# Kernel optimization log

Hardware: AMD Instinct MI355X
Metric: run time of the kernel (lower is better)

Reference implementation:

```python
import jax, jax.numpy as jnp
import numpy as np

B, T = 2, 1023
C, H, HS, L, FF = 1024, 16, 64, 6, 4096
V, BS = 50258, 1024


def setup_inputs() -> dict:
    key = jax.random.key(0)
    ks = iter(jax.random.split(key, 80))
    def w(shape):
        return 0.02 * jax.random.normal(next(ks), shape, dtype=jnp.float32)
    inp = {}
    inp['x'] = jax.random.randint(next(ks), (B, T), 0, V)
    inp['y'] = jax.random.randint(next(ks), (B, T), 0, V)
    inp['wte'] = w((V, C))
    inp['wpe_x'] = w((BS, C))
    inp['wpe_y'] = w((BS, C))
    # encoder blocks (stacked over L layers)
    inp['enc_Wq'] = w((L, H, C, HS)); inp['enc_Wk'] = w((L, H, C, HS)); inp['enc_Wv'] = w((L, H, C, HS))
    inp['enc_pw'] = w((L, C, C)); inp['enc_pb'] = jnp.zeros((L, C), jnp.float32)
    inp['enc_ln1g'] = jnp.ones((L, C), jnp.float32); inp['enc_ln1b'] = jnp.zeros((L, C), jnp.float32)
    inp['enc_ln2g'] = jnp.ones((L, C), jnp.float32); inp['enc_ln2b'] = jnp.zeros((L, C), jnp.float32)
    inp['enc_w1'] = w((L, C, FF)); inp['enc_b1'] = jnp.zeros((L, FF), jnp.float32)
    inp['enc_w2'] = w((L, FF, C)); inp['enc_b2'] = jnp.zeros((L, C), jnp.float32)
    # decoder blocks: self-attn (masked), cross-attn, ffn
    inp['dec_sWq'] = w((L, H, C, HS)); inp['dec_sWk'] = w((L, H, C, HS)); inp['dec_sWv'] = w((L, H, C, HS))
    inp['dec_spw'] = w((L, C, C)); inp['dec_spb'] = jnp.zeros((L, C), jnp.float32)
    inp['dec_cWq'] = w((L, H, C, HS)); inp['dec_cWk'] = w((L, H, C, HS)); inp['dec_cWv'] = w((L, H, C, HS))
    inp['dec_cpw'] = w((L, C, C)); inp['dec_cpb'] = jnp.zeros((L, C), jnp.float32)
    inp['dec_ln1g'] = jnp.ones((L, C), jnp.float32); inp['dec_ln1b'] = jnp.zeros((L, C), jnp.float32)
    inp['dec_ln2g'] = jnp.ones((L, C), jnp.float32); inp['dec_ln2b'] = jnp.zeros((L, C), jnp.float32)
    inp['dec_ln3g'] = jnp.ones((L, C), jnp.float32); inp['dec_ln3b'] = jnp.zeros((L, C), jnp.float32)
    inp['dec_w1'] = w((L, C, FF)); inp['dec_b1'] = jnp.zeros((L, FF), jnp.float32)
    inp['dec_w2'] = w((L, FF, C)); inp['dec_b2'] = jnp.zeros((L, C), jnp.float32)
    inp['lnf_g'] = jnp.ones((C,), jnp.float32); inp['lnf_b'] = jnp.zeros((C,), jnp.float32)
    inp['lm_b'] = jnp.zeros((V,), jnp.float32)  # lm_head weight tied to wte
    return inp


def _ln(x, g, b):
    m = x.mean(-1, keepdims=True)
    v = ((x - m) ** 2).mean(-1, keepdims=True)
    return g * (x - m) / jnp.sqrt(v + 1e-5) + b


def _mha(xq, xkv, Wq, Wk, Wv, pw, pb, causal):
    # per-head projections batched over heads: [B,T,C] x [H,C,HS] -> [B,H,T,HS]
    q = jnp.einsum('btc,hcd->bhtd', xq, Wq)
    k = jnp.einsum('bsc,hcd->bhsd', xkv, Wk)
    v = jnp.einsum('bsc,hcd->bhsd', xkv, Wv)
    # NOTE: original scales by sqrt(n_embed) (C from x.size()), not sqrt(head_size)
    s = jnp.einsum('bhtd,bhsd->bhts', q, k) / jnp.sqrt(jnp.float32(C))
    if causal:
        mask = jnp.tril(jnp.ones((xq.shape[1], xkv.shape[1]), bool))
        s = jnp.where(mask, s, -jnp.inf)
    a = jax.nn.softmax(s, axis=-1)
    o = jnp.einsum('bhts,bhsd->bhtd', a, v)
    o = o.transpose(0, 2, 1, 3).reshape(xq.shape[0], xq.shape[1], H * HS)
    return o @ pw + pb


def _ffn(x, w1, b1, w2, b2):
    return jnp.maximum(x @ w1 + b1, 0.0) @ w2 + b2


def _forward(x, y, p):
    enc = p['wte'][x] + p['wpe_x'][:x.shape[1]]
    for i in range(L):
        enc = enc + _ln(_mha(enc, enc, p['enc_Wq'][i], p['enc_Wk'][i], p['enc_Wv'][i], p['enc_pw'][i], p['enc_pb'][i], False), p['enc_ln1g'][i], p['enc_ln1b'][i])
        enc = enc + _ln(_ffn(enc, p['enc_w1'][i], p['enc_b1'][i], p['enc_w2'][i], p['enc_b2'][i]), p['enc_ln2g'][i], p['enc_ln2b'][i])
    dec = p['wte'][y] + p['wpe_y'][:y.shape[1]]
    for i in range(L):
        dec = dec + _ln(_mha(dec, dec, p['dec_sWq'][i], p['dec_sWk'][i], p['dec_sWv'][i], p['dec_spw'][i], p['dec_spb'][i], True), p['dec_ln1g'][i], p['dec_ln1b'][i])
        dec = dec + _ln(_mha(dec, enc, p['dec_cWq'][i], p['dec_cWk'][i], p['dec_cWv'][i], p['dec_cpw'][i], p['dec_cpb'][i], False), p['dec_ln2g'][i], p['dec_ln2b'][i])
        dec = dec + _ln(_ffn(dec, p['dec_w1'][i], p['dec_b1'][i], p['dec_w2'][i], p['dec_b2'][i]), p['dec_ln3g'][i], p['dec_ln3b'][i])
    dec = _ln(dec, p['lnf_g'], p['lnf_b'])
    return dec @ p['wte'].T + p['lm_b']


def reference(x, y, wte, wpe_x, wpe_y,
              enc_Wq, enc_Wk, enc_Wv, enc_pw, enc_pb, enc_ln1g, enc_ln1b, enc_ln2g, enc_ln2b,
              enc_w1, enc_b1, enc_w2, enc_b2,
              dec_sWq, dec_sWk, dec_sWv, dec_spw, dec_spb,
              dec_cWq, dec_cWk, dec_cWv, dec_cpw, dec_cpb,
              dec_ln1g, dec_ln1b, dec_ln2g, dec_ln2b, dec_ln3g, dec_ln3b,
              dec_w1, dec_b1, dec_w2, dec_b2,
              lnf_g, lnf_b, lm_b):
    p = dict(wte=wte, wpe_x=wpe_x, wpe_y=wpe_y,
             enc_Wq=enc_Wq, enc_Wk=enc_Wk, enc_Wv=enc_Wv, enc_pw=enc_pw, enc_pb=enc_pb,
             enc_ln1g=enc_ln1g, enc_ln1b=enc_ln1b, enc_ln2g=enc_ln2g, enc_ln2b=enc_ln2b,
             enc_w1=enc_w1, enc_b1=enc_b1, enc_w2=enc_w2, enc_b2=enc_b2,
             dec_sWq=dec_sWq, dec_sWk=dec_sWk, dec_sWv=dec_sWv, dec_spw=dec_spw, dec_spb=dec_spb,
             dec_cWq=dec_cWq, dec_cWk=dec_cWk, dec_cWv=dec_cWv, dec_cpw=dec_cpw, dec_cpb=dec_cpb,
             dec_ln1g=dec_ln1g, dec_ln1b=dec_ln1b, dec_ln2g=dec_ln2g, dec_ln2b=dec_ln2b,
             dec_ln3g=dec_ln3g, dec_ln3b=dec_ln3b,
             dec_w1=dec_w1, dec_b1=dec_b1, dec_w2=dec_w2, dec_b2=dec_b2,
             lnf_g=lnf_g, lnf_b=lnf_b, lm_b=lm_b)
    return _forward(x, y, p)
```

## Files before the change

kernel.cpp:

```cpp
#include <hip/hip_runtime.h>
#include <hip/hip_bf16.h>

#define BB 2
#define TT 1023
#define CC 1024
#define HH 16
#define HSZ 64
#define LL 6
#define FFD 4096
#define VV 50258
#define MM (BB*TT)
#define MP 2048
#define VP 50304

typedef __attribute__((ext_vector_type(4))) float  f32x4;
typedef __attribute__((ext_vector_type(8))) short  s16x8;
typedef __attribute__((ext_vector_type(4))) short  s16x4;

#define SCHED0   __builtin_amdgcn_sched_barrier(0)
#define SBAR     __builtin_amdgcn_s_barrier()
#define LGKMCNT0 asm volatile("s_waitcnt lgkmcnt(0)" ::: "memory")

__device__ __forceinline__ short f2b(float x) {
    __hip_bfloat16 h = __float2bfloat16(x);
    short s;
    __builtin_memcpy(&s, &h, 2);
    return s;
}

__device__ __forceinline__ void gld16(const void* g, void* l) {
    __builtin_amdgcn_global_load_lds(
        (__attribute__((address_space(1))) const void*)g,
        (__attribute__((address_space(3))) void*)l, 16, 0, 0);
}

__global__ __launch_bounds__(256) void embed_kernel(
    const int* __restrict__ ids, const float* __restrict__ wte,
    const float* __restrict__ wpe, float* __restrict__ out,
    __hip_bfloat16* __restrict__ outb)
{
    int r = blockIdx.x;
    int t = r % TT;
    long id = ids[r];
    int c = threadIdx.x * 4;
    float4 a = *(const float4*)(wte + id * (long)CC + c);
    float4 p = *(const float4*)(wpe + (long)t * CC + c);
    float4 o; o.x = a.x + p.x; o.y = a.y + p.y; o.z = a.z + p.z; o.w = a.w + p.w;
    *(float4*)(out + (long)r * CC + c) = o;
    s16x4 h; h[0] = f2b(o.x); h[1] = f2b(o.y); h[2] = f2b(o.z); h[3] = f2b(o.w);
    *(s16x4*)(outb + (long)r * CC + c) = h;
}

__global__ __launch_bounds__(256) void cvtb_kernel(
    const float* __restrict__ in, __hip_bfloat16* __restrict__ out, long n)
{
    long i = ((long)blockIdx.x * 256 + threadIdx.x) * 8;
    if (i >= n) return;
    float4 f0 = *(const float4*)(in + i);
    float4 f1 = *(const float4*)(in + i + 4);
    s16x8 h;
    h[0]=f2b(f0.x); h[1]=f2b(f0.y); h[2]=f2b(f0.z); h[3]=f2b(f0.w);
    h[4]=f2b(f1.x); h[5]=f2b(f1.y); h[6]=f2b(f1.z); h[7]=f2b(f1.w);
    *(s16x8*)(out + i) = h;
}

__global__ __launch_bounds__(256) void tcvt_kernel(
    const float* __restrict__ in, __hip_bfloat16* __restrict__ out,
    int R, int S, long inZ, long outZa, long outZb, int zdiv)
{
    int z = blockIdx.z;
    in  += (long)z * inZ;
    out += (long)(z / zdiv) * outZa + (long)(z % zdiv) * outZb;
    __shared__ float tile[32][33];
    int s0 = blockIdx.x * 32, r0 = blockIdx.y * 32;
    int tx = threadIdx.x, ty = threadIdx.y;
    #pragma unroll
    for (int i = 0; i < 4; ++i)
        tile[ty + i * 8][tx] = in[(long)(r0 + ty + i * 8) * S + s0 + tx];
    __syncthreads();
    #pragma unroll
    for (int i = 0; i < 4; ++i)
        out[(long)(s0 + ty + i * 8) * R + r0 + tx] =
            __float2bfloat16(tile[tx][ty + i * 8]);
}

template<int WMODE, bool RELU, bool B64>
__global__ __launch_bounds__(256) void mgemm2_kernel(
    const __hip_bfloat16* __restrict__ A, const __hip_bfloat16* __restrict__ B,
    const float* __restrict__ bias, float* __restrict__ Cm,
    __hip_bfloat16* __restrict__ Cb,
    int M, int N, int K, int ldc, int GM)
{
    constexpr int BM   = B64 ? 64 : 128;
    constexpr int ASZ  = BM * 32;
    constexpr int BSZ  = 128 * 32;
    constexpr int BUF  = ASZ + BSZ;
    constexpr int WROW = BM / 2;
    constexpr int NI   = WROW / 16;
    constexpr int NAC  = BM / 64;
    __shared__ short LDS[3 * BUF];

    const int nwg = gridDim.x;
    const int bid = blockIdx.x;
    const int q = nwg >> 3, r = nwg & 7;
    const int xcd = bid & 7, lid = bid >> 3;
    const int swz = (xcd < r) ? xcd * (q + 1) + lid
                              : r * (q + 1) + (xcd - r) * q + lid;
    const int m0 = (swz % GM) * BM;
    const int n0 = (swz / GM) * 128;

    const int tid  = threadIdx.x;
    const int lane = tid & 63, w = tid >> 6;
    const int wr = w >> 1, wc = w & 1;
    const int lr = lane & 15, kg = lane >> 4;

    const __hip_bfloat16* Abase = A + (long)m0 * K;
    const __hip_bfloat16* Bbase = B + (long)n0 * K;

    f32x4 acc[NI][4];
    #pragma unroll
    for (int i = 0; i < NI; ++i)
        #pragma unroll
        for (int j = 0; j < 4; ++j)
            acc[i][j] = (f32x4){0.f, 0.f, 0.f, 0.f};

    const int srow = lane >> 2;
    const int scol = (((lane & 3) ^ ((lane >> 3) & 3))) * 8;

    auto stage = [&](int db, long kofs) {
        short* Ad = &LDS[db * BUF];
        short* Bd = Ad + ASZ;
        #pragma unroll
        for (int p = 0; p < NAC; ++p) {
            int cc = p * 4 + w;
            long ro = (long)(cc * 16 + srow) * K + kofs + scol;
            gld16(Abase + ro, Ad + cc * 512);
        }
        #pragma unroll
        for (int p = 0; p < 2; ++p) {
            int cc = p * 4 + w;
            long ro = (long)(cc * 16 + srow) * K + kofs + scol;
            gld16(Bbase + ro, Bd + cc * 512);
        }
    };
    const int rslot = (kg ^ ((lr >> 1) & 3)) * 8;

    auto compute = [&](int db) {
        const short* Ar = &LDS[db * BUF];
        const short* Br = Ar + ASZ;
        s16x8 af[NI], bf[4];
        #pragma unroll
        for (int i = 0; i < NI; ++i)
            af[i] = *(const s16x8*)&Ar[(wr * WROW + i * 16 + lr) * 32 + rslot];
        #pragma unroll
        for (int j = 0; j < 4; ++j)
            bf[j] = *(const s16x8*)&Br[(wc * 64 + j * 16 + lr) * 32 + rslot];
        __builtin_amdgcn_s_setprio(1);
        #pragma unroll
        for (int i = 0; i < NI; ++i)
            #pragma unroll
            for (int j = 0; j < 4; ++j)
                acc[i][j] = __builtin_amdgcn_mfma_f32_16x16x32_bf16(
                    af[i], bf[j], acc[i][j], 0, 0, 0);
        __builtin_amdgcn_s_setprio(0);
    };

    const int nt = K >> 5;
    stage(0, 0);
    if (nt > 1) stage(1, 32);
    int db = 0;
    for (int t = 0; t < nt; ++t) {
        if (t + 2 < nt) {
            stage((db + 2) % 3, (long)(t + 2) << 5);
            SCHED0;
            if (B64) asm volatile("s_waitcnt vmcnt(6)" ::: "memory");
            else     asm volatile("s_waitcnt vmcnt(8)" ::: "memory");
            SCHED0;
        } else if (t + 1 < nt) {
            SCHED0;
            if (B64) asm volatile("s_waitcnt vmcnt(3)" ::: "memory");
            else     asm volatile("s_waitcnt vmcnt(4)" ::: "memory");
            SCHED0;
        } else {
            SCHED0; asm volatile("s_waitcnt vmcnt(0)" ::: "memory"); SCHED0;
        }
        SBAR; SCHED0;
        compute(db);
        SCHED0; LGKMCNT0; SCHED0; SBAR; SCHED0;
        db = (db + 1) % 3;
    }

    if (WMODE == 0) {
        float* LF = (float*)&LDS[0];
        if (!B64) {
            #pragma unroll
            for (int h = 0; h < 2; ++h) {
                if (wc == h) {
                    #pragma unroll
                    for (int j = 0; j < 4; ++j) {
                        int gcol = n0 + h * 64 + j * 16 + lr;
                        float bv = (bias && gcol < N) ? bias[gcol] : 0.f;
                        #pragma unroll
                        for (int i = 0; i < NI; ++i) {
                            int row0 = wr * WROW + i * 16 + kg * 4;
                            #pragma unroll
                            for (int qq = 0; qq < 4; ++qq) {
                                float v = acc[i][j][qq] + bv;
                                if (RELU) v = fmaxf(v, 0.f);
                                LF[(row0 + qq) * 64 + j * 16 + lr] = v;
                            }
                        }
                    }
                }
                __syncthreads();
                #pragma unroll
                for (int i = 0; i < 16; ++i) {
                    int F = i * 256 + tid;
                    int row = F >> 5, col = (F & 31) * 2;
                    int gr = m0 + row, gc = n0 + h * 64 + col;
                    if (gr < M && gc < N)
                        *(float2*)(Cm + (long)gr * ldc + gc) = *(const float2*)&LF[row * 64 + col];
                }
                __syncthreads();
            }
        } else {
            #pragma unroll
            for (int j = 0; j < 4; ++j) {
                int gcol = n0 + wc * 64 + j * 16 + lr;
                float bv = (bias && gcol < N) ? bias[gcol] : 0.f;
                #pragma unroll
                for (int i = 0; i < NI; ++i) {
                    int row0 = wr * WROW + i * 16 + kg * 4;
                    #pragma unroll
                    for (int qq = 0; qq < 4; ++qq) {
                        float v = acc[i][j][qq] + bv;
                        if (RELU) v = fmaxf(v, 0.f);
                        LF[(row0 + qq) * 128 + wc * 64 + j * 16 + lr] = v;
                    }
                }
            }
            __syncthreads();
            #pragma unroll
            for (int i = 0; i < 16; ++i) {
                int F = i * 256 + tid;
                int row = F >> 6, col = (F & 63) * 2;
                int gr = m0 + row, gc = n0 + col;
                if (gr < M && gc < N)
                    *(float2*)(Cm + (long)gr * ldc + gc) = *(const float2*)&LF[row * 128 + col];
            }
        }
    } else {
        short* LS = (short*)&LDS[0];
        #pragma unroll
        for (int j = 0; j < 4; ++j) {
            int gcol = n0 + wc * 64 + j * 16 + lr;
            float bv = (bias && gcol < N) ? bias[gcol] : 0.f;
            #pragma unroll
            for (int i = 0; i < NI; ++i) {
                int row0 = wr * WROW + i * 16 + kg * 4;
                #pragma unroll
                for (int qq = 0; qq < 4; ++qq) {
                    float v = acc[i][j][qq] + bv;
                    if (RELU) v = fmaxf(v, 0.f);
                    LS[(row0 + qq) * 128 + wc * 64 + j * 16 + lr] = f2b(v);
                }
            }
        }
        __syncthreads();
        #pragma unroll
        for (int i = 0; i < BM / 16; ++i) {
            int F = i * 256 + tid;
            int row = F >> 4, col = (F & 15) * 8;
            int gr = m0 + row, gc = n0 + col;
            if (gr < M && gc < N)
                *(s16x8*)((short*)Cb + (long)gr * ldc + gc) = *(const s16x8*)&LS[row * 128 + col];
        }
    }
}

__global__ __launch_bounds__(256) void mgemm_f32b_kernel(
    const float* __restrict__ A, const float* __restrict__ Bv,
    const float* __restrict__ bias, float* __restrict__ Cm,
    int M, int N, int K, int ldc)
{
    __shared__ short As[128][40];
    __shared__ short Bs[128][40];
    const int tid  = threadIdx.x;
    const int lane = tid & 63, w = tid >> 6;
    const int wr = w >> 1, wc = w & 1;
    const int lr = lane & 15, kg = lane >> 4;
    const int m0 = blockIdx.y * 128, n0 = blockIdx.x * 128;
    const int ar = tid >> 3, ac = (tid & 7) * 4;
    const int br = tid >> 2, bc = (tid & 3) * 8;

    f32x4 acc[4][4];
    #pragma unroll
    for (int i = 0; i < 4; ++i)
        #pragma unroll
        for (int j = 0; j < 4; ++j)
            acc[i][j] = (f32x4){0.f, 0.f, 0.f, 0.f};

    for (int k0 = 0; k0 < K; k0 += 32) {
        #pragma unroll
        for (int p = 0; p < 4; ++p) {
            int row = ar + p * 32, gm = m0 + row;
            float4 f = {0.f, 0.f, 0.f, 0.f};
            if (gm < M) f = *(const float4*)(A + (long)gm * K + k0 + ac);
            s16x4 h; h[0] = f2b(f.x); h[1] = f2b(f.y); h[2] = f2b(f.z); h[3] = f2b(f.w);
            *(s16x4*)&As[row][ac] = h;
        }
        #pragma unroll
        for (int p = 0; p < 2; ++p) {
            int n = br + p * 64, gn = n0 + n;
            s16x8 h = (s16x8){0,0,0,0,0,0,0,0};
            if (gn < N) {
                float4 f0 = *(const float4*)(Bv + (long)gn * K + k0 + bc);
                float4 f1 = *(const float4*)(Bv + (long)gn * K + k0 + bc + 4);
                h[0]=f2b(f0.x); h[1]=f2b(f0.y); h[2]=f2b(f0.z); h[3]=f2b(f0.w);
                h[4]=f2b(f1.x); h[5]=f2b(f1.y); h[6]=f2b(f1.z); h[7]=f2b(f1.w);
            }
            *(s16x8*)&Bs[n][bc] = h;
        }
        __syncthreads();
        s16x8 af[4], bf[4];
        #pragma unroll
        for (int i = 0; i < 4; ++i) af[i] = *(const s16x8*)&As[wr*64 + i*16 + lr][kg*8];
        #pragma unroll
        for (int j = 0; j < 4; ++j) bf[j] = *(const s16x8*)&Bs[wc*64 + j*16 + lr][kg*8];
        #pragma unroll
        for (int i = 0; i < 4; ++i)
            #pragma unroll
            for (int j = 0; j < 4; ++j)
                acc[i][j] = __builtin_amdgcn_mfma_f32_16x16x32_bf16(af[i], bf[j], acc[i][j], 0, 0, 0);
        __syncthreads();
    }
    #pragma unroll
    for (int j = 0; j < 4; ++j) {
        int gcol = n0 + wc * 64 + j * 16 + lr;
        if (gcol >= N) continue;
        float bv = bias ? bias[gcol] : 0.f;
        #pragma unroll
        for (int i = 0; i < 4; ++i) {
            int grow0 = m0 + wr * 64 + i * 16 + kg * 4;
            #pragma unroll
            for (int qq = 0; qq < 4; ++qq) {
                int gr = grow0 + qq;
                if (gr >= M) continue;
                Cm[(long)gr * ldc + gcol] = acc[i][j][qq] + bv;
            }
        }
    }
}

template<bool CAUSAL>
__global__ __launch_bounds__(256) void fattn_kernel(
    const __hip_bfloat16* __restrict__ qkvb, __hip_bfloat16* __restrict__ outb)
{
    __shared__ short Ks[128][72];
    __shared__ short Vt[64][136];
    __shared__ short Ps[4][16][136];

    const int q0 = blockIdx.x * 64;
    const int h = blockIdx.y, b = blockIdx.z;
    const int tid = threadIdx.x;
    const int lane = tid & 63, w = tid >> 6;
    const int lr = lane & 15, lg = lane >> 4;

    const float scale = 1.0f / 32.0f;
    const long base = (long)b * TT * 3072;
    const __hip_bfloat16* Kg = qkvb + base + 1024 + h * 64;
    const __hip_bfloat16* Vg = qkvb + base + 2048 + h * 64;

    s16x8 qf[2];
    {
        int qr = q0 + w * 16 + lr;
        #pragma unroll
        for (int kc = 0; kc < 2; ++kc) {
            s16x8 hv = (s16x8){0,0,0,0,0,0,0,0};
            if (qr < TT)
                hv = *(const s16x8*)(qkvb + base + (long)qr * 3072 + h * 64 + kc * 32 + lg * 8);
            qf[kc] = hv;
        }
    }

    f32x4 acc[4];
    #pragma unroll
    for (int jd = 0; jd < 4; ++jd) acc[jd] = (f32x4){0.f, 0.f, 0.f, 0.f};
    float mrun[4] = {-3.0e38f, -3.0e38f, -3.0e38f, -3.0e38f};
    float lrun[4] = {0.f, 0.f, 0.f, 0.f};

    const int send = CAUSAL ? min(TT, q0 + 64) : TT;
    const int nt = (send + 127) >> 7;
    const int sr4 = (tid >> 3) * 4;
    const int dcc = (tid & 7) * 8;

    s16x8 kreg[4], vreg[4];
    auto loadkv = [&](int t) {
        int sbase = t * 128;
        #pragma unroll
        for (int rr = 0; rr < 4; ++rr) {
            int sg = sbase + sr4 + rr;
            if (sg < TT) {
                kreg[rr] = *(const s16x8*)(Kg + (long)sg * 3072 + dcc);
                vreg[rr] = *(const s16x8*)(Vg + (long)sg * 3072 + dcc);
            } else {
                kreg[rr] = (s16x8){0,0,0,0,0,0,0,0};
                vreg[rr] = (s16x8){0,0,0,0,0,0,0,0};
            }
        }
    };

    loadkv(0);
    for (int ti = 0; ti < nt; ++ti) {
        const int s0 = ti * 128;
        SCHED0; SBAR; SCHED0;
        #pragma unroll
        for (int rr = 0; rr < 4; ++rr)
            *(s16x8*)&Ks[sr4 + rr][dcc] = kreg[rr];
        #pragma unroll
        for (int pr = 0; pr < 2; ++pr) {
            #pragma unroll
            for (int e = 0; e < 8; ++e) {
                unsigned pack = (unsigned)(unsigned short)vreg[2*pr][e]
                              | ((unsigned)(unsigned short)vreg[2*pr + 1][e] << 16);
                *(unsigned*)&Vt[dcc + e][sr4 + 2*pr] = pack;
            }
        }
        if (ti + 1 < nt) loadkv(ti + 1);
        SCHED0; LGKMCNT0; SCHED0; SBAR; SCHED0;

        f32x4 sf[8];
        __builtin_amdgcn_s_setprio(1);
        #pragma unroll
        for (int j = 0; j < 8; ++j) {
            f32x4 z = (f32x4){0.f, 0.f, 0.f, 0.f};
            #pragma unroll
            for (int kc = 0; kc < 2; ++kc) {
                s16x8 kf = *(const s16x8*)&Ks[j * 16 + lr][kc * 32 + lg * 8];
                z = __builtin_amdgcn_mfma_f32_16x16x32_bf16(qf[kc], kf, z, 0, 0, 0);
            }
            sf[j] = z;
        }
        __builtin_amdgcn_s_setprio(0);

        float mloc[4] = {-3.0e38f, -3.0e38f, -3.0e38f, -3.0e38f};
        #pragma unroll
        for (int j = 0; j < 8; ++j) {
            int sg = s0 + j * 16 + lr;
            #pragma unroll
            for (int r = 0; r < 4; ++r) {
                float sc = sf[j][r] * scale;
                int qg = q0 + w * 16 + lg * 4 + r;
                if ((CAUSAL && sg > qg) || sg >= TT) sc = -3.0e38f;
                sf[j][r] = sc;
                mloc[r] = fmaxf(mloc[r], sc);
            }
        }
        #pragma unroll
        for (int r = 0; r < 4; ++r)
            #pragma unroll
            for (int off = 1; off < 16; off <<= 1)
                mloc[r] = fmaxf(mloc[r], __shfl_xor(mloc[r], off));

        float corr[4], psum[4];
        #pragma unroll
        for (int r = 0; r < 4; ++r) {
            float mn = fmaxf(mrun[r], mloc[r]);
            corr[r] = __expf(mrun[r] - mn);
            mrun[r] = mn;
            psum[r] = 0.f;
        }

        #pragma unroll
        for (int j = 0; j < 8; ++j) {
            #pragma unroll
            for (int r = 0; r < 4; ++r) {
                float p = __expf(sf[j][r] - mrun[r]);
                psum[r] += p;
                Ps[w][lg * 4 + r][j * 16 + lr] = f2b(p);
            }
        }
        #pragma unroll
        for (int r = 0; r < 4; ++r) {
            #pragma unroll
            for (int off = 1; off < 16; off <<= 1)
                psum[r] += __shfl_xor(psum[r], off);
            lrun[r] = lrun[r] * corr[r] + psum[r];
            #pragma unroll
            for (int jd = 0; jd < 4; ++jd) acc[jd][r] *= corr[r];
        }

        __builtin_amdgcn_s_setprio(1);
        #pragma unroll
        for (int kc = 0; kc < 4; ++kc) {
            s16x8 pa = *(const s16x8*)&Ps[w][lr][kc * 32 + lg * 8];
            #pragma unroll
            for (int jd = 0; jd < 4; ++jd) {
                s16x8 bv = *(const s16x8*)&Vt[jd * 16 + lr][kc * 32 + lg * 8];
                acc[jd] = __builtin_amdgcn_mfma_f32_16x16x32_bf16(pa, bv, acc[jd], 0, 0, 0);
            }
        }
        __builtin_amdgcn_s_setprio(0);
        SCHED0; LGKMCNT0; SCHED0;
    }

    #pragma unroll
    for (int r = 0; r < 4; ++r) {
        int qg = q0 + w * 16 + lg * 4 + r;
        if (qg >= TT) continue;
        float inv = 1.0f / lrun[r];
        #pragma unroll
        for (int jd = 0; jd < 4; ++jd)
            outb[((long)b * TT + qg) * CC + h * 64 + jd * 16 + lr] =
                __float2bfloat16(acc[jd][r] * inv);
    }
}

__global__ __launch_bounds__(256) void ln_kernel(
    const float* __restrict__ in, const float* __restrict__ res,
    const float* __restrict__ g, const float* __restrict__ b,
    float* __restrict__ out, __hip_bfloat16* __restrict__ outb)
{
    const int r = blockIdx.x, tid = threadIdx.x;
    __shared__ float sm[4];

    float4 xv = *(const float4*)(in + (long)r * CC + tid * 4);
    float s = xv.x + xv.y + xv.z + xv.w;
    #pragma unroll
    for (int o = 32; o > 0; o >>= 1) s += __shfl_xor(s, o);
    if ((tid & 63) == 0) sm[tid >> 6] = s;
    __syncthreads();
    const float mean = (sm[0] + sm[1] + sm[2] + sm[3]) * (1.0f / CC);
    __syncthreads();

    float4 d; d.x = xv.x - mean; d.y = xv.y - mean; d.z = xv.z - mean; d.w = xv.w - mean;
    float s2 = d.x * d.x + d.y * d.y + d.z * d.z + d.w * d.w;
    #pragma unroll
    for (int o = 32; o > 0; o >>= 1) s2 += __shfl_xor(s2, o);
    if ((tid & 63) == 0) sm[tid >> 6] = s2;
    __syncthreads();
    const float rstd = rsqrtf((sm[0] + sm[1] + sm[2] + sm[3]) * (1.0f / CC) + 1e-5f);

    float4 gv = *(const float4*)(g + tid * 4);
    float4 bv = *(const float4*)(b + tid * 4);
    float4 o;
    o.x = gv.x * d.x * rstd + bv.x; o.y = gv.y * d.y * rstd + bv.y;
    o.z = gv.z * d.z * rstd + bv.z; o.w = gv.w * d.w * rstd + bv.w;
    if (res) {
        float4 rv = *(const float4*)(res + (long)r * CC + tid * 4);
        o.x += rv.x; o.y += rv.y; o.z += rv.z; o.w += rv.w;
    }
    *(float4*)(out + (long)r * CC + tid * 4) = o;
    if (outb) {
        s16x4 h; h[0] = f2b(o.x); h[1] = f2b(o.y); h[2] = f2b(o.z); h[3] = f2b(o.w);
        *(s16x4*)(outb + (long)r * CC + tid * 4) = h;
    }
}

extern "C" void kernel_launch(void* const* d_in, const int* in_sizes, int n_in,
                              void* d_out, int out_size, void* d_ws, size_t ws_size,
                              hipStream_t stream)
{
    const int*   x      = (const int*)  d_in[0];
    const int*   y      = (const int*)  d_in[1];
    const float* wte    = (const float*)d_in[2];
    const float* wpe_x  = (const float*)d_in[3];
    const float* wpe_y  = (const float*)d_in[4];
    const float* eWq    = (const float*)d_in[5];
    const float* eWk    = (const float*)d_in[6];
    const float* eWv    = (const float*)d_in[7];
    const float* epw    = (const float*)d_in[8];
    const float* epb    = (const float*)d_in[9];
    const float* eln1g  = (const float*)d_in[10];
    const float* eln1b  = (const float*)d_in[11];
    const float* eln2g  = (const float*)d_in[12];
    const float* eln2b  = (const float*)d_in[13];
    const float* ew1    = (const float*)d_in[14];
    const float* eb1    = (const float*)d_in[15];
    const float* ew2    = (const float*)d_in[16];
    const float* eb2    = (const float*)d_in[17];
    const float* dsWq   = (const float*)d_in[18];
    const float* dsWk   = (const float*)d_in[19];
    const float* dsWv   = (const float*)d_in[20];
    const float* dspw   = (const float*)d_in[21];
    const float* dspb   = (const float*)d_in[22];
    const float* dcWq   = (const float*)d_in[23];
    const float* dcWk   = (const float*)d_in[24];
    const float* dcWv   = (const float*)d_in[25];
    const float* dcpw   = (const float*)d_in[26];
    const float* dcpb   = (const float*)d_in[27];
    const float* dln1g  = (const float*)d_in[28];
    const float* dln1b  = (const float*)d_in[29];
    const float* dln2g  = (const float*)d_in[30];
    const float* dln2b  = (const float*)d_in[31];
    const float* dln3g  = (const float*)d_in[32];
    const float* dln3b  = (const float*)d_in[33];
    const float* dw1    = (const float*)d_in[34];
    const float* db1    = (const float*)d_in[35];
    const float* dw2    = (const float*)d_in[36];
    const float* db2    = (const float*)d_in[37];
    const float* lnfg   = (const float*)d_in[38];
    const float* lnfb   = (const float*)d_in[39];
    const float* lm_b   = (const float*)d_in[40];

    float* out = (float*)d_out;

    const size_t MCp = (size_t)MP * CC;
    float* enc = (float*)d_ws;
    float* dec = enc + MCp;
    float* t0  = dec + MCp;
    __hip_bfloat16* encb = (__hip_bfloat16*)(t0 + MCp);
    __hip_bfloat16* decb = encb + MCp;
    __hip_bfloat16* t0b  = decb + MCp;
    __hip_bfloat16* a0b  = t0b + MCp;
    __hip_bfloat16* qkvb = a0b + MCp;
    __hip_bfloat16* ffb  = qkvb + (size_t)MP * 3072;
    __hip_bfloat16* wteb = ffb + (size_t)MP * FFD;
    __hip_bfloat16* eQKVw = wteb + (size_t)VP * CC;
    __hip_bfloat16* ePWw  = eQKVw + (size_t)LL * 3072 * CC;
    __hip_bfloat16* eW1w  = ePWw  + (size_t)LL * CC * CC;
    __hip_bfloat16* eW2w  = eW1w  + (size_t)LL * FFD * CC;
    __hip_bfloat16* sQKVw = eW2w  + (size_t)LL * CC * FFD;
    __hip_bfloat16* sPWw  = sQKVw + (size_t)LL * 3072 * CC;
    __hip_bfloat16* cQKVw = sPWw  + (size_t)LL * CC * CC;
    __hip_bfloat16* cPWw  = cQKVw + (size_t)LL * 3072 * CC;
    __hip_bfloat16* dW1w  = cPWw  + (size_t)LL * CC * CC;
    __hip_bfloat16* dW2w  = dW1w  + (size_t)LL * FFD * CC;
    __hip_bfloat16* bigEnd = dW2w + (size_t)LL * CC * FFD;
    __hip_bfloat16* wb = eQKVw;
    const size_t needBig   = (size_t)((char*)bigEnd - (char*)d_ws);
    const size_t needSmall = (size_t)((char*)(wb + (size_t)FFD * CC) - (char*)d_ws);
    const size_t needWteb  = (size_t)((char*)eQKVw - (char*)d_ws);
    const bool big     = (ws_size >= needBig);
    const bool useWteb = (ws_size >= needWteb) &&
                         (big || ws_size >= needSmall);

    const int QT = (TT + 63) / 64;
    const dim3 tblk(32, 8);

    auto gemm = [&](const __hip_bfloat16* A, const __hip_bfloat16* B,
                    const float* bias, float* Cm, __hip_bfloat16* Cb,
                    int N_, int K_, int ldc, int wmode, bool relu) {
        const bool b64 = (N_ <= 2048);
        const int GMv = b64 ? MP / 64 : MP / 128;
        int nwg = GMv * ((N_ + 127) / 128);
        if (wmode == 0) {
            if (b64) {
                if (relu) mgemm2_kernel<0, true , true ><<<nwg, 256, 0, stream>>>(A, B, bias, Cm, Cb, MM, N_, K_, ldc, GMv);
                else      mgemm2_kernel<0, false, true ><<<nwg, 256, 0, stream>>>(A, B, bias, Cm, Cb, MM, N_, K_, ldc, GMv);
            } else {
                if (relu) mgemm2_kernel<0, true , false><<<nwg, 256, 0, stream>>>(A, B, bias, Cm, Cb, MM, N_, K_, ldc, GMv);
                else      mgemm2_kernel<0, false, false><<<nwg, 256, 0, stream>>>(A, B, bias, Cm, Cb, MM, N_, K_, ldc, GMv);
            }
        } else {
            if (b64) {
                if (relu) mgemm2_kernel<2, true , true ><<<nwg, 256, 0, stream>>>(A, B, bias, Cm, Cb, MM, N_, K_, ldc, GMv);
                else      mgemm2_kernel<2, false, true ><<<nwg, 256, 0, stream>>>(A, B, bias, Cm, Cb, MM, N_, K_, ldc, GMv);
            } else {
                if (relu) mgemm2_kernel<2, true , false><<<nwg, 256, 0, stream>>>(A, B, bias, Cm, Cb, MM, N_, K_, ldc, GMv);
                else      mgemm2_kernel<2, false, false><<<nwg, 256, 0, stream>>>(A, B, bias, Cm, Cb, MM, N_, K_, ldc, GMv);
            }
        }
    };

    if (useWteb) {
        long n = (long)VV * CC;
        cvtb_kernel<<<(int)((n / 8 + 255) / 256), 256, 0, stream>>>(wte, wteb, n);
    }

    if (big) {
        const long sWH = (long)CC * HSZ;
        const long oA = (long)3072 * CC;
        const long oB = (long)HSZ * CC;
        dim3 gq(HSZ / 32, CC / 32, LL * HH);
        tcvt_kernel<<<gq, tblk, 0, stream>>>(eWq, eQKVw,             CC, HSZ, sWH, oA, oB, HH);
        tcvt_kernel<<<gq, tblk, 0, stream>>>(eWk, eQKVw + CC * CC,   CC, HSZ, sWH, oA, oB, HH);
        tcvt_kernel<<<gq, tblk, 0, stream>>>(eWv, eQKVw + 2*CC*CC,   CC, HSZ, sWH, oA, oB, HH);
        tcvt_kernel<<<gq, tblk, 0, stream>>>(dsWq, sQKVw,            CC, HSZ, sWH, oA, oB, HH);
        tcvt_kernel<<<gq, tblk, 0, stream>>>(dsWk, sQKVw + CC * CC,  CC, HSZ, sWH, oA, oB, HH);
        tcvt_kernel<<<gq, tblk, 0, stream>>>(dsWv, sQKVw + 2*CC*CC,  CC, HSZ, sWH, oA, oB, HH);
        tcvt_kernel<<<gq, tblk, 0, stream>>>(dcWq, cQKVw,            CC, HSZ, sWH, oA, oB, HH);
        tcvt_kernel<<<gq, tblk, 0, stream>>>(dcWk, cQKVw + CC * CC,  CC, HSZ, sWH, oA, oB, HH);
        tcvt_kernel<<<gq, tblk, 0, stream>>>(dcWv, cQKVw + 2*CC*CC,  CC, HSZ, sWH, oA, oB, HH);
        dim3 gp(CC / 32, CC / 32, LL);
        tcvt_kernel<<<gp, tblk, 0, stream>>>(epw,  ePWw, CC, CC, (long)CC*CC, (long)CC*CC, 0, 1);
        tcvt_kernel<<<gp, tblk, 0, stream>>>(dspw, sPWw, CC, CC, (long)CC*CC, (long)CC*CC, 0, 1);
        tcvt_kernel<<<gp, tblk, 0, stream>>>(dcpw, cPWw, CC, CC, (long)CC*CC, (long)CC*CC, 0, 1);
        dim3 g1(FFD / 32, CC / 32, LL);
        tcvt_kernel<<<g1, tblk, 0, stream>>>(ew1, eW1w, CC, FFD, (long)CC*FFD, (long)FFD*CC, 0, 1);
        tcvt_kernel<<<g1, tblk, 0, stream>>>(dw1, dW1w, CC, FFD, (long)CC*FFD, (long)FFD*CC, 0, 1);
        dim3 g2(CC / 32, FFD / 32, LL);
        tcvt_kernel<<<g2, tblk, 0, stream>>>(ew2, eW2w, FFD, CC, (long)FFD*CC, (long)CC*FFD, 0, 1);
        tcvt_kernel<<<g2, tblk, 0, stream>>>(dw2, dW2w, FFD, CC, (long)FFD*CC, (long)CC*FFD, 0, 1);
    }

    auto cvt_qkv = [&](const float* Wq, const float* Wk, const float* Wv) {
        dim3 g(HSZ / 32, CC / 32, HH);
        tcvt_kernel<<<g, tblk, 0, stream>>>(Wq, wb,             CC, HSZ, (long)CC*HSZ, (long)HSZ*CC, 0, 1);
        tcvt_kernel<<<g, tblk, 0, stream>>>(Wk, wb + CC*CC,     CC, HSZ, (long)CC*HSZ, (long)HSZ*CC, 0, 1);
        tcvt_kernel<<<g, tblk, 0, stream>>>(Wv, wb + 2*CC*CC,   CC, HSZ, (long)CC*HSZ, (long)HSZ*CC, 0, 1);
    };
    auto cvt_nt = [&](const float* W, int R, int S) {
        dim3 g(S / 32, R / 32, 1);
        tcvt_kernel<<<g, tblk, 0, stream>>>(W, wb, R, S, 0, 0, 0, 1);
    };

    embed_kernel<<<MM, 256, 0, stream>>>(x, wte, wpe_x, enc, encb);
    for (int i = 0; i < LL; ++i) {
        const long cOff = (long)i * CC;
        const __hip_bfloat16 *Wqkv, *Wp, *W1, *W2;
        if (big) {
            Wqkv = eQKVw + (size_t)i * 3072 * CC;
            Wp   = ePWw  + (size_t)i * CC * CC;
            W1   = eW1w  + (size_t)i * FFD * CC;
            W2   = eW2w  + (size_t)i * CC * FFD;
        }
        if (!big) cvt_qkv(eWq + (long)i*HH*CC*HSZ, eWk + (long)i*HH*CC*HSZ, eWv + (long)i*HH*CC*HSZ), Wqkv = wb;
        gemm(encb, Wqkv, nullptr, nullptr, qkvb, 3072, CC, 3072, 2, false);
        fattn_kernel<false><<<dim3(QT, HH, BB), 256, 0, stream>>>(qkvb, a0b);
        if (!big) cvt_nt(epw + (long)i*CC*CC, CC, CC), Wp = wb;
        gemm(a0b, Wp, epb + cOff, t0, nullptr, CC, CC, CC, 0, false);
        ln_kernel<<<MM, 256, 0, stream>>>(t0, enc, eln1g + cOff, eln1b + cOff, enc, encb);
        if (!big) cvt_nt(ew1 + (long)i*CC*FFD, CC, FFD), W1 = wb;
        gemm(encb, W1, eb1 + (long)i*FFD, nullptr, ffb, FFD, CC, FFD, 2, true);
        if (!big) cvt_nt(ew2 + (long)i*FFD*CC, FFD, CC), W2 = wb;
        gemm(ffb, W2, eb2 + cOff, t0, nullptr, CC, FFD, CC, 0, false);
        ln_kernel<<<MM, 256, 0, stream>>>(t0, enc, eln2g + cOff, eln2b + cOff, enc, encb);
    }

    embed_kernel<<<MM, 256, 0, stream>>>(y, wte, wpe_y, dec, decb);
    for (int i = 0; i < LL; ++i) {
        const long cOff = (long)i * CC;
        const __hip_bfloat16 *Ws, *Wsp, *Wc, *Wcp, *W1, *W2;
        if (big) {
            Ws  = sQKVw + (size_t)i * 3072 * CC;
            Wsp = sPWw  + (size_t)i * CC * CC;
            Wc  = cQKVw + (size_t)i * 3072 * CC;
            Wcp = cPWw  + (size_t)i * CC * CC;
            W1  = dW1w  + (size_t)i * FFD * CC;
            W2  = dW2w  + (size_t)i * CC * FFD;
        }
        if (!big) cvt_qkv(dsWq + (long)i*HH*CC*HSZ, dsWk + (long)i*HH*CC*HSZ, dsWv + (long)i*HH*CC*HSZ), Ws = wb;
        gemm(decb, Ws, nullptr, nullptr, qkvb, 3072, CC, 3072, 2, false);
        fattn_kernel<true><<<dim3(QT, HH, BB), 256, 0, stream>>>(qkvb, a0b);
        if (!big) cvt_nt(dspw + (long)i*CC*CC, CC, CC), Wsp = wb;
        gemm(a0b, Wsp, dspb + cOff, t0, nullptr, CC, CC, CC, 0, false);
        ln_kernel<<<MM, 256, 0, stream>>>(t0, dec, dln1g + cOff, dln1b + cOff, dec, decb);
        if (!big) cvt_qkv(dcWq + (long)i*HH*CC*HSZ, dcWk + (long)i*HH*CC*HSZ, dcWv + (long)i*HH*CC*HSZ), Wc = wb;
        gemm(decb, Wc, nullptr, nullptr, qkvb, CC, CC, 3072, 2, false);
        gemm(encb, Wc + (size_t)CC * CC, nullptr, nullptr, qkvb + CC, 2048, CC, 3072, 2, false);
        fattn_kernel<false><<<dim3(QT, HH, BB), 256, 0, stream>>>(qkvb, a0b);
        if (!big) cvt_nt(dcpw + (long)i*CC*CC, CC, CC), Wcp = wb;
        gemm(a0b, Wcp, dcpb + cOff, t0, nullptr, CC, CC, CC, 0, false);
        ln_kernel<<<MM, 256, 0, stream>>>(t0, dec, dln2g + cOff, dln2b + cOff, dec, decb);
        if (!big) cvt_nt(dw1 + (long)i*CC*FFD, CC, FFD), W1 = wb;
        gemm(decb, W1, db1 + (long)i*FFD, nullptr, ffb, FFD, CC, FFD, 2, true);
        if (!big) cvt_nt(dw2 + (long)i*FFD*CC, FFD, CC), W2 = wb;
        gemm(ffb, W2, db2 + cOff, t0, nullptr, CC, FFD, CC, 0, false);
        ln_kernel<<<MM, 256, 0, stream>>>(t0, dec, dln3g + cOff, dln3b + cOff, dec, decb);
    }

    ln_kernel<<<MM, 256, 0, stream>>>(dec, nullptr, lnfg, lnfb, t0, t0b);
    if (useWteb) {
        const int GMv = 1024 / 128;
        const int nwg = GMv * ((VV + 127) / 128);
        mgemm2_kernel<0, false, false><<<nwg, 256, 0, stream>>>(
            t0b, wteb, lm_b, out, nullptr, 1024, VV, CC, VV, GMv);
        mgemm2_kernel<0, false, false><<<nwg, 256, 0, stream>>>(
            t0b + (size_t)1024 * CC, wteb, lm_b, out + (size_t)1024 * VV, nullptr,
            MM - 1024, VV, CC, VV, GMv);
    } else {
        dim3 grid((VV + 127) / 128, MP / 128);
        mgemm_f32b_kernel<<<grid, 256, 0, stream>>>(t0, wte, lm_b, out, MM, VV, CC, VV);
    }
}
```

Baseline: 3.127 ms.

## Store pre-LN GEMM outputs as bf16, pre-scale Q, and lazily rescale softmax

The projection and FFN-down GEMMs now write bf16 instead of fp32, and a new layer-norm kernel reads that bf16 input, which halves the traffic for the intermediate activation. In flash attention the 1/32 scale is folded into Q once at load time. The online-softmax rescale of the accumulators now runs only when some row's max grows by more than a threshold, which skips the exp and multiply work on most tiles. The costs are a bf16 rounding of the residual-branch output before layer norm, an extra bf16 rounding of the scaled Q, and exp values that may exceed 1 while the running max lags.

After: 3.093 ms. About the same (-1.1%).

```diff
diff --git a/kernel.cpp b/kernel.cpp
--- a/kernel.cpp
+++ b/kernel.cpp
@@ -26,6 +26,12 @@
     short s;
     __builtin_memcpy(&s, &h, 2);
     return s;
+}
+__device__ __forceinline__ float b2f(short s) {
+    unsigned u = ((unsigned)(unsigned short)s) << 16;
+    float f;
+    __builtin_memcpy(&f, &u, 4);
+    return f;
 }
 
 __device__ __forceinline__ void gld16(const void* g, void* l) {
@@ -366,7 +372,6 @@
     const int lane = tid & 63, w = tid >> 6;
     const int lr = lane & 15, lg = lane >> 4;
 
-    const float scale = 1.0f / 32.0f;
     const long base = (long)b * TT * 3072;
     const __hip_bfloat16* Kg = qkvb + base + 1024 + h * 64;
     const __hip_bfloat16* Vg = qkvb + base + 2048 + h * 64;
@@ -377,8 +382,12 @@
         #pragma unroll
         for (int kc = 0; kc < 2; ++kc) {
             s16x8 hv = (s16x8){0,0,0,0,0,0,0,0};
-            if (qr < TT)
+            if (qr < TT) {
                 hv = *(const s16x8*)(qkvb + base + (long)qr * 3072 + h * 64 + kc * 32 + lg * 8);
+                #pragma unroll
+                for (int e = 0; e < 8; ++e)
+                    hv[e] = f2b(b2f(hv[e]) * 0.03125f);
+            }
             qf[kc] = hv;
         }
     }
@@ -449,7 +458,7 @@
             int sg = s0 + j * 16 + lr;
             #pragma unroll
             for (int r = 0; r < 4; ++r) {
-                float sc = sf[j][r] * scale;
+                float sc = sf[j][r];
                 int qg = q0 + w * 16 + lg * 4 + r;
                 if ((CAUSAL && sg > qg) || sg >= TT) sc = -3.0e38f;
                 sf[j][r] = sc;
@@ -462,15 +471,23 @@
             for (int off = 1; off < 16; off <<= 1)
                 mloc[r] = fmaxf(mloc[r], __shfl_xor(mloc[r], off));
 
-        float corr[4], psum[4];
-        #pragma unroll
-        for (int r = 0; r < 4; ++r) {
-            float mn = fmaxf(mrun[r], mloc[r]);
-            corr[r] = __expf(mrun[r] - mn);
-            mrun[r] = mn;
-            psum[r] = 0.f;
-        }
-
+        bool grow = false;
+        #pragma unroll
+        for (int r = 0; r < 4; ++r)
+            grow = grow || (mloc[r] > mrun[r] + 8.0f);
+        if (__any((int)grow)) {
+            #pragma unroll
+            for (int r = 0; r < 4; ++r) {
+                float mn = fmaxf(mrun[r], mloc[r]);
+                float corr = __expf(mrun[r] - mn);
+                mrun[r] = mn;
+                lrun[r] *= corr;
+                #pragma unroll
+                for (int jd = 0; jd < 4; ++jd) acc[jd][r] *= corr;
+            }
+        }
+
+        float psum[4] = {0.f, 0.f, 0.f, 0.f};
         #pragma unroll
         for (int j = 0; j < 8; ++j) {
             #pragma unroll
@@ -485,9 +502,7 @@
             #pragma unroll
             for (int off = 1; off < 16; off <<= 1)
                 psum[r] += __shfl_xor(psum[r], off);
-            lrun[r] = lrun[r] * corr[r] + psum[r];
-            #pragma unroll
-            for (int jd = 0; jd < 4; ++jd) acc[jd][r] *= corr[r];
+            lrun[r] += psum[r];
         }
 
         __builtin_amdgcn_s_setprio(1);
@@ -555,6 +570,47 @@
         s16x4 h; h[0] = f2b(o.x); h[1] = f2b(o.y); h[2] = f2b(o.z); h[3] = f2b(o.w);
         *(s16x4*)(outb + (long)r * CC + tid * 4) = h;
     }
+}
+
+__global__ __launch_bounds__(256) void lnb_kernel(
+    const __hip_bfloat16* __restrict__ in, const float* __restrict__ res,
+    const float* __restrict__ g, const float* __restrict__ b,
+    float* __restrict__ out, __hip_bfloat16* __restrict__ outb)
+{
+    const int r = blockIdx.x, tid = threadIdx.x;
+    __shared__ float sm[4];
+
+    s16x4 hv = *(const s16x4*)((const short*)in + (long)r * CC + tid * 4);
+    float4 xv;
+    xv.x = b2f(hv[0]); xv.y = b2f(hv[1]); xv.z = b2f(hv[2]); xv.w = b2f(hv[3]);
+    float s = xv.x + xv.y + xv.z + xv.w;
+    #pragma unroll
+    for (int o = 32; o > 0; o >>= 1) s += __shfl_xor(s, o);
+    if ((tid & 63) == 0) sm[tid >> 6] = s;
+    __syncthreads();
+    const float mean = (sm[0] + sm[1] + sm[2] + sm[3]) * (1.0f / CC);
+    __syncthreads();
+
+    float4 d; d.x = xv.x - mean; d.y = xv.y - mean; d.z = xv.z - mean; d.w = xv.w - mean;
+    float s2 = d.x * d.x + d.y * d.y + d.z * d.z + d.w * d.w;
+    #pragma unroll
+    for (int o = 32; o > 0; o >>= 1) s2 += __shfl_xor(s2, o);
+    if ((tid & 63) == 0) sm[tid >> 6] = s2;
+    __syncthreads();
+    const float rstd = rsqrtf((sm[0] + sm[1] + sm[2] + sm[3]) * (1.0f / CC) + 1e-5f);
+
+    float4 gv = *(const float4*)(g + tid * 4);
+    float4 bv = *(const float4*)(b + tid * 4);
+    float4 o;
+    o.x = gv.x * d.x * rstd + bv.x; o.y = gv.y * d.y * rstd + bv.y;
+    o.z = gv.z * d.z * rstd + bv.z; o.w = gv.w * d.w * rstd + bv.w;
+    if (res) {
+        float4 rv = *(const float4*)(res + (long)r * CC + tid * 4);
+        o.x += rv.x; o.y += rv.y; o.z += rv.z; o.w += rv.w;
+    }
+    *(float4*)(out + (long)r * CC + tid * 4) = o;
+    s16x4 hh; hh[0] = f2b(o.x); hh[1] = f2b(o.y); hh[2] = f2b(o.z); hh[3] = f2b(o.w);
+    *(s16x4*)((short*)outb + (long)r * CC + tid * 4) = hh;
 }
 
 extern "C" void kernel_launch(void* const* d_in, const int* in_sizes, int n_in,
@@ -719,13 +775,13 @@
         gemm(encb, Wqkv, nullptr, nullptr, qkvb, 3072, CC, 3072, 2, false);
         fattn_kernel<false><<<dim3(QT, HH, BB), 256, 0, stream>>>(qkvb, a0b);
         if (!big) cvt_nt(epw + (long)i*CC*CC, CC, CC), Wp = wb;
-        gemm(a0b, Wp, epb + cOff, t0, nullptr, CC, CC, CC, 0, false);
-        ln_kernel<<<MM, 256, 0, stream>>>(t0, enc, eln1g + cOff, eln1b + cOff, enc, encb);
+        gemm(a0b, Wp, epb + cOff, nullptr, t0b, CC, CC, CC, 2, false);
+        lnb_kernel<<<MM, 256, 0, stream>>>(t0b, enc, eln1g + cOff, eln1b + cOff, enc, encb);
         if (!big) cvt_nt(ew1 + (long)i*CC*FFD, CC, FFD), W1 = wb;
         gemm(encb, W1, eb1 + (long)i*FFD, nullptr, ffb, FFD, CC, FFD, 2, true);
         if (!big) cvt_nt(ew2 + (long)i*FFD*CC, FFD, CC), W2 = wb;
-        gemm(ffb, W2, eb2 + cOff, t0, nullptr, CC, FFD, CC, 0, false);
-        ln_kernel<<<MM, 256, 0, stream>>>(t0, enc, eln2g + cOff, eln2b + cOff, enc, encb);
+        gemm(ffb, W2, eb2 + cOff, nullptr, t0b, CC, FFD, CC, 2, false);
+        lnb_kernel<<<MM, 256, 0, stream>>>(t0b, enc, eln2g + cOff, eln2b + cOff, enc, encb);
     }
 
     embed_kernel<<<MM, 256, 0, stream>>>(y, wte, wpe_y, dec, decb);
@@ -744,20 +800,20 @@
         gemm(decb, Ws, nullptr, nullptr, qkvb, 3072, CC, 3072, 2, false);
         fattn_kernel<true><<<dim3(QT, HH, BB), 256, 0, stream>>>(qkvb, a0b);
         if (!big) cvt_nt(dspw + (long)i*CC*CC, CC, CC), Wsp = wb;
-        gemm(a0b, Wsp, dspb + cOff, t0, nullptr, CC, CC, CC, 0, false);
-        ln_kernel<<<MM, 256, 0, stream>>>(t0, dec, dln1g + cOff, dln1b + cOff, dec, decb);
+        gemm(a0b, Wsp, dspb + cOff, nullptr, t0b, CC, CC, CC, 2, false);
+        lnb_kernel<<<MM, 256, 0, stream>>>(t0b, dec, dln1g + cOff, dln1b + cOff, dec, decb);
         if (!big) cvt_qkv(dcWq + (long)i*HH*CC*HSZ, dcWk + (long)i*HH*CC*HSZ, dcWv + (long)i*HH*CC*HSZ), Wc = wb;
         gemm(decb, Wc, nullptr, nullptr, qkvb, CC, CC, 3072, 2, false);
         gemm(encb, Wc + (size_t)CC * CC, nullptr, nullptr, qkvb + CC, 2048, CC, 3072, 2, false);
         fattn_kernel<false><<<dim3(QT, HH, BB), 256, 0, stream>>>(qkvb, a0b);
         if (!big) cvt_nt(dcpw + (long)i*CC*CC, CC, CC), Wcp = wb;
-        gemm(a0b, Wcp, dcpb + cOff, t0, nullptr, CC, CC, CC, 0, false);
-        ln_kernel<<<MM, 256, 0, stream>>>(t0, dec, dln2g + cOff, dln2b + cOff, dec, decb);
+        gemm(a0b, Wcp, dcpb + cOff, nullptr, t0b, CC, CC, CC, 2, false);
+        lnb_kernel<<<MM, 256, 0, stream>>>(t0b, dec, dln2g + cOff, dln2b + cOff, dec, decb);
         if (!big) cvt_nt(dw1 + (long)i*CC*FFD, CC, FFD), W1 = wb;
         gemm(decb, W1, db1 + (long)i*FFD, nullptr, ffb, FFD, CC, FFD, 2, true);
         if (!big) cvt_nt(dw2 + (long)i*FFD*CC, FFD, CC), W2 = wb;
-        gemm(ffb, W2, db2 + cOff, t0, nullptr, CC, FFD, CC, 0, false);
-        ln_kernel<<<MM, 256, 0, stream>>>(t0, dec, dln3g + cOff, dln3b + cOff, dec, decb);
+        gemm(ffb, W2, db2 + cOff, nullptr, t0b, CC, FFD, CC, 2, false);
+        lnb_kernel<<<MM, 256, 0, stream>>>(t0b, dec, dln3g + cOff, dln3b + cOff, dec, decb);
     }
 
     ln_kernel<<<MM, 256, 0, stream>>>(dec, nullptr, lnfg, lnfb, t0, t0b);
```
